# Kernel tuning notes

Measured on AMD Instinct MI355X. Metric: run time of the kernel, lower is better.

The kernel has to match this reference:

```python
import jax, jax.numpy as jnp
import numpy as np

# aero table grids (degrees)
A_LO, A_HI = -20.0, 90.0
B_LO, B_HI = -30.0, 30.0
E_LO, E_HI = -25.0, 25.0


def _idx(x, lo, hi, n):
    t = jnp.clip((x - lo) / (hi - lo) * (n - 1), 0.0, float(n - 1))
    i0 = jnp.clip(t.astype(jnp.int32), 0, n - 2)
    return i0, t - i0


def _interp1(tab, x, lo, hi):
    i0, f = _idx(x, lo, hi, tab.shape[-1])
    return tab[..., i0] * (1.0 - f) + tab[..., i0 + 1] * f


def _interp2(tab, a, b):
    ia, fa = _idx(a, A_LO, A_HI, tab.shape[-2])
    ib, fb = _idx(b, B_LO, B_HI, tab.shape[-1])
    return (tab[:, ia, ib] * (1 - fa) * (1 - fb)
            + tab[:, ia + 1, ib] * fa * (1 - fb)
            + tab[:, ia, ib + 1] * (1 - fa) * fb
            + tab[:, ia + 1, ib + 1] * fa * fb)


def _interp3(tab, a, b, e):
    ia, fa = _idx(a, A_LO, A_HI, tab.shape[-3])
    ib, fb = _idx(b, B_LO, B_HI, tab.shape[-2])
    ie, fe = _idx(e, E_LO, E_HI, tab.shape[-1])
    out = 0.0
    for di, wa in ((0, 1 - fa), (1, fa)):
        for dj, wb in ((0, 1 - fb), (1, fb)):
            for dk, we in ((0, 1 - fe), (1, fe)):
                out = out + tab[:, ia + di, ib + dj, ie + dk] * (wa * wb * we)
    return out


def _nlplant(xu, tab3, tab2, tab1, tab_eta):
    g, m, Bspan, S, cbar = 32.17, 636.94, 30.0, 300.0, 11.32
    xcgr, xcg, Heng = 0.35, 0.25, 0.0
    Jy, Jxz, Jz, Jx = 55814.0, 982.0, 63100.0, 9496.0
    r2d = 180.0 / np.pi

    alt = xu[:, 2]
    phi, theta, psi = xu[:, 3], xu[:, 4], xu[:, 5]
    vt = jnp.maximum(xu[:, 6], 0.01)          # if vt < 0.01: vt = 0.01
    alpha, beta = xu[:, 7], xu[:, 8]
    a_deg, b_deg = alpha * r2d, beta * r2d
    P, Q, R = xu[:, 9], xu[:, 10], xu[:, 11]
    T, el, ail, rud, lef = xu[:, 12], xu[:, 13], xu[:, 14], xu[:, 15], xu[:, 16]
    dail, drud, dlef = ail / 21.5, rud / 30.0, 1.0 - lef / 25.0

    # --- Atmos ---
    tfac = 1.0 - 7.03e-06 * alt
    temp = jnp.where(alt >= 35000.0, 390.0, 519.0 * tfac)
    rho = 0.002377 * jnp.power(tfac, 4.14)
    qbar = 0.5 * rho * vt * vt
    ps = 1715.0 * rho * temp
    ps = jnp.where(ps == 0.0, 1715.0, ps)

    sa, ca = jnp.sin(alpha), jnp.cos(alpha)
    sb, cb = jnp.sin(beta), jnp.cos(beta)
    st, ct, tt = jnp.sin(theta), jnp.cos(theta), jnp.tan(theta)
    sphi, cphi = jnp.sin(phi), jnp.cos(phi)
    spsi, cpsi = jnp.sin(psi), jnp.cos(psi)

    U, V, W = vt * ca * cb, vt * sb, vt * sa * cb

    xd0 = U * (ct * cpsi) + V * (sphi * cpsi * st - cphi * spsi) + W * (cphi * st * cpsi + sphi * spsi)
    xd1 = U * (ct * spsi) + V * (sphi * spsi * st + cphi * cpsi) + W * (cphi * st * spsi - sphi * cpsi)
    xd2 = U * st - V * (sphi * ct) - W * (cphi * ct)
    xd3 = P + tt * (Q * sphi + R * cphi)
    xd4 = Q * cphi - R * sphi
    xd5 = (Q * sphi + R * cphi) / ct

    # --- aero table lookups ---
    v3 = _interp3(tab3, a_deg, b_deg, el)                    # [5,B]: Cx,Cz,Cm,Cn,Cl at el
    v30 = _interp3(tab3, a_deg, b_deg, jnp.zeros_like(el))   # [5,B]: at el=0
    v2 = _interp2(tab2, a_deg, b_deg)                        # [16,B]
    v1 = _interp1(tab1, a_deg, A_LO, A_HI)                   # [21,B]
    eta_el = _interp1(tab_eta, el, E_LO, E_HI)               # [B]

    Cx, Cz, Cm, Cn, Cl = v3[0], v3[1], v3[2], v3[3], v3[4]
    Cy = v2[0]
    (Cxq, Cyr, Cyp, Czq, Clr, Clp, Cmq, Cnr, Cnp,
     dCxq_lef, dCyr_lef, dCyp_lef, dCzq_lef, dClr_lef, dClp_lef,
     dCmq_lef, dCnr_lef, dCnp_lef, dCnbeta, dClbeta, dCm) = [v1[i] for i in range(21)]

    d_Cx_lef = v2[1] - v30[0]
    d_Cz_lef = v2[2] - v30[1]
    d_Cm_lef = v2[3] - v30[2]
    d_Cy_lef = v2[4] - v2[0]
    d_Cn_lef = v2[5] - v30[3]
    d_Cl_lef = v2[6] - v30[4]
    d_Cy_r30 = v2[7] - v2[0]
    d_Cn_r30 = v2[8] - v30[3]
    d_Cl_r30 = v2[9] - v30[4]
    d_Cy_a20 = v2[10] - v2[0]
    d_Cy_a20_lef = v2[11] - v2[4]
    d_Cn_a20 = v2[12] - v30[3]
    d_Cn_a20_lef = v2[13] - v2[5]
    d_Cl_a20 = v2[14] - v30[4]
    d_Cl_a20_lef = v2[15] - v2[6]
    d_Cm_ds = 0.0

    # --- total coefficients ---
    c2v = 1.0 / (2.0 * vt)
    dXdQ = cbar * c2v * (Cxq + dCxq_lef * dlef)
    Cx_tot = Cx + d_Cx_lef * dlef + dXdQ * Q
    dZdQ = cbar * c2v * (Czq + dCzq_lef * dlef)
    Cz_tot = Cz + d_Cz_lef * dlef + dZdQ * Q
    dMdQ = cbar * c2v * (Cmq + dCmq_lef * dlef)
    Cm_tot = Cm * eta_el + Cz_tot * (xcgr - xcg) + d_Cm_lef * dlef + dMdQ * Q + dCm + d_Cm_ds
    dYdail = d_Cy_a20 + d_Cy_a20_lef * dlef
    dYdR = Bspan * c2v * (Cyr + dCyr_lef * dlef)
    dYdP = Bspan * c2v * (Cyp + dCyp_lef * dlef)
    Cy_tot = Cy + d_Cy_lef * dlef + dYdail * dail + d_Cy_r30 * drud + dYdR * R + dYdP * P
    dNdail = d_Cn_a20 + d_Cn_a20_lef * dlef
    dNdR = Bspan * c2v * (Cnr + dCnr_lef * dlef)
    dNdP = Bspan * c2v * (Cnp + dCnp_lef * dlef)
    Cn_tot = (Cn + d_Cn_lef * dlef - Cy_tot * (xcgr - xcg) * (cbar / Bspan)
              + dNdail * dail + d_Cn_r30 * drud + dNdR * R + dNdP * P + dCnbeta * b_deg)
    dLdail = d_Cl_a20 + d_Cl_a20_lef * dlef
    dLdR = Bspan * c2v * (Clr + dClr_lef * dlef)
    dLdP = Bspan * c2v * (Clp + dClp_lef * dlef)
    Cl_tot = (Cl + d_Cl_lef * dlef + dLdail * dail + d_Cl_r30 * drud
              + dLdR * R + dLdP * P + dClbeta * b_deg)

    # --- body-axis accelerations ---
    qS_m = qbar * S / m
    Udot = R * V - Q * W - g * st + qS_m * Cx_tot + T / m
    Vdot = P * W - R * U + g * ct * sphi + qS_m * Cy_tot
    Wdot = Q * U - P * V + g * ct * cphi + qS_m * Cz_tot
    vt_dot = (U * Udot + V * Vdot + W * Wdot) / vt
    alpha_dot = (U * Wdot - W * Udot) / (U * U + W * W)
    beta_dot = (Vdot * vt - V * vt_dot) / (vt * vt * cb)

    # --- moments ---
    L_tot = Cl_tot * qbar * S * Bspan
    M_tot = Cm_tot * qbar * S * cbar
    N_tot = Cn_tot * qbar * S * Bspan
    denom = Jx * Jz - Jxz * Jxz
    P_dot = (Jz * L_tot + Jxz * N_tot - (Jz * (Jz - Jy) + Jxz * Jxz) * Q * R
             + Jxz * (Jx - Jy + Jz) * P * Q + Jxz * Q * Heng) / denom
    Q_dot = (M_tot + (Jz - Jx) * P * R - Jxz * (P * P - R * R) - R * Heng) / Jy
    R_dot = (Jx * N_tot + Jxz * L_tot + (Jx * (Jx - Jy) + Jxz * Jxz) * P * Q
             - Jxz * (Jx - Jy + Jz) * Q * R + Jx * Q * Heng) / denom

    xdot12 = jnp.stack([xd0, xd1, xd2, xd3, xd4, xd5,
                        vt_dot, alpha_dot, beta_dot, P_dot, Q_dot, R_dot], axis=1)
    return jnp.concatenate([xdot12, jnp.zeros((xu.shape[0], 5), xu.dtype)], axis=1)


def setup_inputs() -> dict:
    key = jax.random.key(0)
    k0, k1, k2, k3, k4 = jax.random.split(key, 5)
    Bn = 1 << 20
    u = jax.random.uniform(k0, (Bn, 17), dtype=jnp.float32)
    lo = jnp.array([0., 0., 0., -1., -1., -3., 300., -0.30, -0.5, -2., -2., -2.,
                    1000., -25., -21.5, -30., 0.], dtype=jnp.float32)
    hi = jnp.array([1000., 1000., 40000., 1., 1., 3., 900., 0.75, 0.5, 2., 2., 2.,
                    19000., 25., 21.5, 30., 25.], dtype=jnp.float32)
    xu = lo + u * (hi - lo)
    tab3 = 0.1 * jax.random.normal(k1, (5, 20, 19, 5), dtype=jnp.float32)
    tab2 = 0.05 * jax.random.normal(k2, (16, 20, 19), dtype=jnp.float32)
    tab1 = 0.1 * jax.random.normal(k3, (21, 20), dtype=jnp.float32)
    tab_eta = 1.0 + 0.05 * jax.random.normal(k4, (5,), dtype=jnp.float32)
    return {"xu": xu, "tab3": tab3, "tab2": tab2, "tab1": tab1, "tab_eta": tab_eta}


def reference(xu, tab3, tab2, tab1, tab_eta):
    return _nlplant(xu, tab3, tab2, tab1, tab_eta)
```

## Files before the change

### kernel.cpp

```cpp
#include <hip/hip_runtime.h>

#define BLOCK 1024
#define ROWS_PER_BLOCK 1024

__device__ __forceinline__ void idx_of(float x, float lo, float inv_range_times_nm1,
                                       int n, int& i0, float& f) {
    float t = (x - lo) * inv_range_times_nm1;
    t = fminf(fmaxf(t, 0.0f), (float)(n - 1));
    int i = (int)t;
    if (i > n - 2) i = n - 2;
    i0 = i;
    f = t - (float)i;
}

__global__ __launch_bounds__(BLOCK, 1)
void nlplant_kernel(const float* __restrict__ xu,
                    const float* __restrict__ tab3,
                    const float* __restrict__ tab2,
                    const float* __restrict__ tab1,
                    const float* __restrict__ tab_eta,
                    float* __restrict__ out, int nrows)
{
    __shared__ __align__(16) float s_t3a[1900 * 4];
    __shared__ __align__(16) float s_t3b[1900];
    __shared__ __align__(16) float s_tab2[380 * 20];
    __shared__ __align__(16) float s_tab1[20 * 21];
    __shared__ __align__(16) float s_eta[8];
    __shared__ __align__(16) float s_io[512 * 17];

    const int tid = threadIdx.x;

    for (int k = tid; k < 9500; k += BLOCK) {
        int ie = k % 5; int r = k / 5;
        int ib = r % 19; r /= 19;
        int ia = r % 20; int c = r / 20;
        const int idx = (ia * 19 + ib) * 5 + ie;
        const float v = tab3[k];
        if (c < 4) s_t3a[(idx << 2) + c] = v;
        else       s_t3b[idx] = v;
    }
    for (int k = tid; k < 6080; k += BLOCK) {
        int ib = k % 19; int r = k / 19;
        int ia = r % 20; int c = r / 20;
        s_tab2[(ia * 19 + ib) * 20 + c] = tab2[k];
    }
    for (int k = tid; k < 420; k += BLOCK) {
        int ia = k % 20; int c = k / 20;
        s_tab1[ia * 21 + c] = tab1[k];
    }
    if (tid < 5) s_eta[tid] = tab_eta[tid];

    const int base = blockIdx.x * ROWS_PER_BLOCK;
    int remA = nrows - base;           if (remA < 0) remA = 0;
    const int rowsA = remA < 512 ? remA : 512;
    int remB = nrows - base - 512;     if (remB < 0) remB = 0;
    const int rowsB = remB < 512 ? remB : 512;

    if (rowsA == 512) {
        const float4* src = reinterpret_cast<const float4*>(xu + (size_t)base * 17);
        float4* dst = reinterpret_cast<float4*>(s_io);
        for (int k = tid; k < 2176; k += BLOCK) dst[k] = src[k];
    } else {
        for (int k = tid; k < rowsA * 17; k += BLOCK) s_io[k] = xu[(size_t)base * 17 + k];
    }
    __syncthreads();

    const int half = tid >> 9;
    const int l = tid & 511;
    const bool active = (half == 0) ? (l < rowsA) : (l < rowsB);

    float x[17];
#pragma unroll
    for (int j = 0; j < 17; ++j) x[j] = 1.0f;

    if (half == 0 && l < rowsA) {
#pragma unroll
        for (int j = 0; j < 17; ++j) x[j] = s_io[l * 17 + j];
    }
    __syncthreads();

    if (rowsB == 512) {
        const float4* src = reinterpret_cast<const float4*>(xu + (size_t)(base + 512) * 17);
        float4* dst = reinterpret_cast<float4*>(s_io);
        for (int k = tid; k < 2176; k += BLOCK) dst[k] = src[k];
    } else {
        for (int k = tid; k < rowsB * 17; k += BLOCK) s_io[k] = xu[(size_t)(base + 512) * 17 + k];
    }
    __syncthreads();
    if (half == 1 && l < rowsB) {
#pragma unroll
        for (int j = 0; j < 17; ++j) x[j] = s_io[l * 17 + j];
    }

    const float g = 32.17f, m_ = 636.94f, Bs = 30.0f, S = 300.0f, cbar = 11.32f;
    const float xcgr = 0.35f, xcg = 0.25f;
    const float Jy = 55814.0f, Jxz = 982.0f, Jz = 63100.0f, Jx = 9496.0f;
    const float r2d = 57.29577951308232f;

    const float alt = x[2], phi = x[3], theta = x[4], psi = x[5];
    const float vt = fmaxf(x[6], 0.01f);
    const float alpha = x[7], beta = x[8];
    const float a_deg = alpha * r2d, b_deg = beta * r2d;
    const float P = x[9], Q = x[10], R = x[11];
    const float T = x[12], el = x[13], ail = x[14], rud = x[15], lef = x[16];

    const float dail = ail * (1.0f / 21.5f);
    const float drud = rud * (1.0f / 30.0f);
    const float dlef = 1.0f - lef * (1.0f / 25.0f);

    const float tfac = 1.0f - 7.03e-6f * alt;
    const float rho = 0.002377f * __expf(4.14f * __logf(tfac));
    const float qbar = 0.5f * rho * vt * vt;

    float sa, ca, sb, cb, st, ct, sphi, cphi, spsi, cpsi;
    __sincosf(alpha, &sa, &ca);
    __sincosf(beta, &sb, &cb);
    __sincosf(theta, &st, &ct);
    __sincosf(phi, &sphi, &cphi);
    __sincosf(psi, &spsi, &cpsi);
    const float tt = st / ct;

    int ia, ib, ie; float fa, fb, fe;
    idx_of(a_deg, -20.0f, 19.0f / 110.0f, 20, ia, fa);
    idx_of(b_deg, -30.0f, 18.0f / 60.0f, 19, ib, fb);
    idx_of(el,    -25.0f,  4.0f / 50.0f,  5, ie, fe);

    const float wa[2] = {1.0f - fa, fa};
    const float wb[2] = {1.0f - fb, fb};
    const float we[2] = {1.0f - fe, fe};

    float v3c[5]  = {0, 0, 0, 0, 0};
    float v30c[5] = {0, 0, 0, 0, 0};
#pragma unroll
    for (int di = 0; di < 2; ++di) {
#pragma unroll
        for (int dj = 0; dj < 2; ++dj) {
            const float wab = wa[di] * wb[dj];
            const int pb = ((ia + di) * 19 + (ib + dj)) * 5;
#pragma unroll
            for (int dk = 0; dk < 2; ++dk) {
                const int idx = pb + ie + dk;
                const float4 q = *reinterpret_cast<const float4*>(&s_t3a[idx << 2]);
                const float q4 = s_t3b[idx];
                const float w = wab * we[dk];
                v3c[0] += q.x * w; v3c[1] += q.y * w; v3c[2] += q.z * w;
                v3c[3] += q.w * w; v3c[4] += q4 * w;
            }
            const int zidx = pb + 2;
            const float4 q0 = *reinterpret_cast<const float4*>(&s_t3a[zidx << 2]);
            const float q04 = s_t3b[zidx];
            v30c[0] += q0.x * wab; v30c[1] += q0.y * wab; v30c[2] += q0.z * wab;
            v30c[3] += q0.w * wab; v30c[4] += q04 * wab;
        }
    }

    float v2c[16];
    {
        const float w00 = wa[0] * wb[0], w01 = wa[0] * wb[1];
        const float w10 = wa[1] * wb[0], w11 = wa[1] * wb[1];
        const float4* p00 = reinterpret_cast<const float4*>(&s_tab2[(ia * 19 + ib) * 20]);
        const float4* p01 = reinterpret_cast<const float4*>(&s_tab2[(ia * 19 + ib + 1) * 20]);
        const float4* p10 = reinterpret_cast<const float4*>(&s_tab2[((ia + 1) * 19 + ib) * 20]);
        const float4* p11 = reinterpret_cast<const float4*>(&s_tab2[((ia + 1) * 19 + ib + 1) * 20]);
#pragma unroll
        for (int q = 0; q < 4; ++q) {
            const float4 a = p00[q], b = p01[q], c = p10[q], d = p11[q];
            v2c[4 * q + 0] = a.x * w00 + b.x * w01 + c.x * w10 + d.x * w11;
            v2c[4 * q + 1] = a.y * w00 + b.y * w01 + c.y * w10 + d.y * w11;
            v2c[4 * q + 2] = a.z * w00 + b.z * w01 + c.z * w10 + d.z * w11;
            v2c[4 * q + 3] = a.w * w00 + b.w * w01 + c.w * w10 + d.w * w11;
        }
    }

    float v1c[21];
    {
        const float* r0 = &s_tab1[ia * 21];
        const float* r1 = &s_tab1[(ia + 1) * 21];
#pragma unroll
        for (int c = 0; c < 21; ++c) v1c[c] = r0[c] * wa[0] + r1[c] * wa[1];
    }
    const float eta_el = s_eta[ie] * we[0] + s_eta[ie + 1] * we[1];

    const float Cx = v3c[0], Cz = v3c[1], Cm = v3c[2], Cn = v3c[3], Cl = v3c[4];
    const float Cy = v2c[0];
    const float Cxq = v1c[0], Cyr = v1c[1], Cyp = v1c[2], Czq = v1c[3], Clr = v1c[4];
    const float Clp = v1c[5], Cmq = v1c[6], Cnr = v1c[7], Cnp = v1c[8];
    const float dCxq_lef = v1c[9], dCyr_lef = v1c[10], dCyp_lef = v1c[11];
    const float dCzq_lef = v1c[12], dClr_lef = v1c[13], dClp_lef = v1c[14];
    const float dCmq_lef = v1c[15], dCnr_lef = v1c[16], dCnp_lef = v1c[17];
    const float dCnbeta = v1c[18], dClbeta = v1c[19], dCm = v1c[20];

    const float d_Cx_lef = v2c[1] - v30c[0];
    const float d_Cz_lef = v2c[2] - v30c[1];
    const float d_Cm_lef = v2c[3] - v30c[2];
    const float d_Cy_lef = v2c[4] - v2c[0];
    const float d_Cn_lef = v2c[5] - v30c[3];
    const float d_Cl_lef = v2c[6] - v30c[4];
    const float d_Cy_r30 = v2c[7] - v2c[0];
    const float d_Cn_r30 = v2c[8] - v30c[3];
    const float d_Cl_r30 = v2c[9] - v30c[4];
    const float d_Cy_a20 = v2c[10] - v2c[0];
    const float d_Cy_a20_lef = v2c[11] - v2c[4];
    const float d_Cn_a20 = v2c[12] - v30c[3];
    const float d_Cn_a20_lef = v2c[13] - v2c[5];
    const float d_Cl_a20 = v2c[14] - v30c[4];
    const float d_Cl_a20_lef = v2c[15] - v2c[6];

    const float U = vt * ca * cb, V = vt * sb, W = vt * sa * cb;
    const float o0 = U * (ct * cpsi) + V * (sphi * cpsi * st - cphi * spsi) + W * (cphi * st * cpsi + sphi * spsi);
    const float o1 = U * (ct * spsi) + V * (sphi * spsi * st + cphi * cpsi) + W * (cphi * st * spsi - sphi * cpsi);
    const float o2 = U * st - V * (sphi * ct) - W * (cphi * ct);
    const float o3 = P + tt * (Q * sphi + R * cphi);
    const float o4 = Q * cphi - R * sphi;
    const float o5 = (Q * sphi + R * cphi) / ct;

    const float c2v = 1.0f / (2.0f * vt);
    const float cq = cbar * c2v, bq = Bs * c2v;
    const float dXdQ = cq * (Cxq + dCxq_lef * dlef);
    const float Cx_tot = Cx + d_Cx_lef * dlef + dXdQ * Q;
    const float dZdQ = cq * (Czq + dCzq_lef * dlef);
    const float Cz_tot = Cz + d_Cz_lef * dlef + dZdQ * Q;
    const float dMdQ = cq * (Cmq + dCmq_lef * dlef);
    const float Cm_tot = Cm * eta_el + Cz_tot * (xcgr - xcg) + d_Cm_lef * dlef + dMdQ * Q + dCm;
    const float dYdail = d_Cy_a20 + d_Cy_a20_lef * dlef;
    const float dYdR = bq * (Cyr + dCyr_lef * dlef);
    const float dYdP = bq * (Cyp + dCyp_lef * dlef);
    const float Cy_tot = Cy + d_Cy_lef * dlef + dYdail * dail + d_Cy_r30 * drud + dYdR * R + dYdP * P;
    const float dNdail = d_Cn_a20 + d_Cn_a20_lef * dlef;
    const float dNdR = bq * (Cnr + dCnr_lef * dlef);
    const float dNdP = bq * (Cnp + dCnp_lef * dlef);
    const float Cn_tot = Cn + d_Cn_lef * dlef - Cy_tot * ((xcgr - xcg) * (cbar / Bs))
                       + dNdail * dail + d_Cn_r30 * drud + dNdR * R + dNdP * P + dCnbeta * b_deg;
    const float dLdail = d_Cl_a20 + d_Cl_a20_lef * dlef;
    const float dLdR = bq * (Clr + dClr_lef * dlef);
    const float dLdP = bq * (Clp + dClp_lef * dlef);
    const float Cl_tot = Cl + d_Cl_lef * dlef + dLdail * dail + d_Cl_r30 * drud
                       + dLdR * R + dLdP * P + dClbeta * b_deg;

    const float qS = qbar * S;
    const float qS_m = qS * (1.0f / m_);
    const float Udot = R * V - Q * W - g * st + qS_m * Cx_tot + T * (1.0f / m_);
    const float Vdot = P * W - R * U + g * ct * sphi + qS_m * Cy_tot;
    const float Wdot = Q * U - P * V + g * ct * cphi + qS_m * Cz_tot;
    const float o6 = (U * Udot + V * Vdot + W * Wdot) / vt;
    const float o7 = (U * Wdot - W * Udot) / (U * U + W * W);
    const float o8 = (Vdot * vt - V * o6) / (vt * vt * cb);

    const float L_tot = Cl_tot * qS * Bs;
    const float M_tot = Cm_tot * qS * cbar;
    const float N_tot = Cn_tot * qS * Bs;
    const float denom = Jx * Jz - Jxz * Jxz;
    const float inv_denom = 1.0f / denom;
    const float o9  = (Jz * L_tot + Jxz * N_tot - (Jz * (Jz - Jy) + Jxz * Jxz) * Q * R
                      + Jxz * (Jx - Jy + Jz) * P * Q) * inv_denom;
    const float o10 = (M_tot + (Jz - Jx) * P * R - Jxz * (P * P - R * R)) * (1.0f / Jy);
    const float o11 = (Jx * N_tot + Jxz * L_tot + (Jx * (Jx - Jy) + Jxz * Jxz) * P * Q
                      - Jxz * (Jx - Jy + Jz) * Q * R) * inv_denom;

    float o[17] = {o0, o1, o2, o3, o4, o5, o6, o7, o8, o9, o10, o11,
                   0.0f, 0.0f, 0.0f, 0.0f, 0.0f};

    __syncthreads();
    if (half == 0 && active) {
#pragma unroll
        for (int j = 0; j < 17; ++j) s_io[l * 17 + j] = o[j];
    }
    __syncthreads();
    if (rowsA == 512) {
        const float4* src = reinterpret_cast<const float4*>(s_io);
        float4* dst = reinterpret_cast<float4*>(out + (size_t)base * 17);
        for (int k = tid; k < 2176; k += BLOCK) dst[k] = src[k];
    } else {
        for (int k = tid; k < rowsA * 17; k += BLOCK) out[(size_t)base * 17 + k] = s_io[k];
    }
    __syncthreads();
    if (half == 1 && active) {
#pragma unroll
        for (int j = 0; j < 17; ++j) s_io[l * 17 + j] = o[j];
    }
    __syncthreads();
    if (rowsB == 512) {
        const float4* src = reinterpret_cast<const float4*>(s_io);
        float4* dst = reinterpret_cast<float4*>(out + (size_t)(base + 512) * 17);
        for (int k = tid; k < 2176; k += BLOCK) dst[k] = src[k];
    } else {
        for (int k = tid; k < rowsB * 17; k += BLOCK) out[(size_t)(base + 512) * 17 + k] = s_io[k];
    }
}

extern "C" void kernel_launch(void* const* d_in, const int* in_sizes, int n_in,
                              void* d_out, int out_size, void* d_ws, size_t ws_size,
                              hipStream_t stream) {
    const float* xu      = (const float*)d_in[0];
    const float* tab3    = (const float*)d_in[1];
    const float* tab2    = (const float*)d_in[2];
    const float* tab1    = (const float*)d_in[3];
    const float* tab_eta = (const float*)d_in[4];
    float* out = (float*)d_out;

    const int nrows = in_sizes[0] / 17;
    const int grid = (nrows + ROWS_PER_BLOCK - 1) / ROWS_PER_BLOCK;
    nlplant_kernel<<<grid, BLOCK, 0, stream>>>(xu, tab3, tab2, tab1, tab_eta, out, nrows);
}
```

Baseline: 69.35 us.

## Shrink shared staging to four 256-row phases and swizzle tab2 layout

Cuts the I/O staging buffer from 512 to 256 rows, processed in four phases, and packs tab2 into 16-float rows with a rotation swizzle. The eta table moves into the tab1 buffer. Together these lower LDS use per block, presumably so two blocks can share a CU, and the launch bound is raised to match. The swizzle is meant to cut LDS bank conflicts on the tab2 float4 reads. The cost is twice as many barrier-separated staging phases, so each block spends more time synchronising.

```diff
diff --git a/kernel.cpp b/kernel.cpp
--- a/kernel.cpp
+++ b/kernel.cpp
@@ -2,6 +2,7 @@
 
 #define BLOCK 1024
 #define ROWS_PER_BLOCK 1024
+#define PHASE 256
 
 __device__ __forceinline__ void idx_of(float x, float lo, float inv_range_times_nm1,
                                        int n, int& i0, float& f) {
@@ -13,7 +14,7 @@
     f = t - (float)i;
 }
 
-__global__ __launch_bounds__(BLOCK, 1)
+__global__ __launch_bounds__(BLOCK, 8)
 void nlplant_kernel(const float* __restrict__ xu,
                     const float* __restrict__ tab3,
                     const float* __restrict__ tab2,
@@ -23,10 +24,9 @@
 {
     __shared__ __align__(16) float s_t3a[1900 * 4];
     __shared__ __align__(16) float s_t3b[1900];
-    __shared__ __align__(16) float s_tab2[380 * 20];
-    __shared__ __align__(16) float s_tab1[20 * 21];
-    __shared__ __align__(16) float s_eta[8];
-    __shared__ __align__(16) float s_io[512 * 17];
+    __shared__ __align__(16) float s_tab2[380 * 16];
+    __shared__ __align__(16) float s_tab1[428];
+    __shared__ __align__(16) float s_io[PHASE * 17];
 
     const int tid = threadIdx.x;
 
@@ -42,54 +42,43 @@
     for (int k = tid; k < 6080; k += BLOCK) {
         int ib = k % 19; int r = k / 19;
         int ia = r % 20; int c = r / 20;
-        s_tab2[(ia * 19 + ib) * 20 + c] = tab2[k];
+        const int idx = ia * 19 + ib;
+        const int q = c >> 2, j = c & 3;
+        s_tab2[(idx << 4) + (((q + (idx >> 1)) & 3) << 2) + j] = tab2[k];
     }
     for (int k = tid; k < 420; k += BLOCK) {
         int ia = k % 20; int c = k / 20;
         s_tab1[ia * 21 + c] = tab1[k];
     }
-    if (tid < 5) s_eta[tid] = tab_eta[tid];
+    if (tid < 5) s_tab1[420 + tid] = tab_eta[tid];
 
     const int base = blockIdx.x * ROWS_PER_BLOCK;
-    int remA = nrows - base;           if (remA < 0) remA = 0;
-    const int rowsA = remA < 512 ? remA : 512;
-    int remB = nrows - base - 512;     if (remB < 0) remB = 0;
-    const int rowsB = remB < 512 ? remB : 512;
-
-    if (rowsA == 512) {
-        const float4* src = reinterpret_cast<const float4*>(xu + (size_t)base * 17);
-        float4* dst = reinterpret_cast<float4*>(s_io);
-        for (int k = tid; k < 2176; k += BLOCK) dst[k] = src[k];
-    } else {
-        for (int k = tid; k < rowsA * 17; k += BLOCK) s_io[k] = xu[(size_t)base * 17 + k];
-    }
-    __syncthreads();
-
-    const int half = tid >> 9;
-    const int l = tid & 511;
-    const bool active = (half == 0) ? (l < rowsA) : (l < rowsB);
+    const int own = tid >> 8;
+    const int l = tid & 255;
 
     float x[17];
 #pragma unroll
     for (int j = 0; j < 17; ++j) x[j] = 1.0f;
-
-    if (half == 0 && l < rowsA) {
-#pragma unroll
-        for (int j = 0; j < 17; ++j) x[j] = s_io[l * 17 + j];
-    }
-    __syncthreads();
-
-    if (rowsB == 512) {
-        const float4* src = reinterpret_cast<const float4*>(xu + (size_t)(base + 512) * 17);
-        float4* dst = reinterpret_cast<float4*>(s_io);
-        for (int k = tid; k < 2176; k += BLOCK) dst[k] = src[k];
-    } else {
-        for (int k = tid; k < rowsB * 17; k += BLOCK) s_io[k] = xu[(size_t)(base + 512) * 17 + k];
-    }
-    __syncthreads();
-    if (half == 1 && l < rowsB) {
-#pragma unroll
-        for (int j = 0; j < 17; ++j) x[j] = s_io[l * 17 + j];
+    bool active = false;
+
+    for (int p = 0; p < 4; ++p) {
+        const int pb = base + p * PHASE;
+        int rem = nrows - pb; if (rem < 0) rem = 0;
+        const int rows = rem < PHASE ? rem : PHASE;
+        if (rows == PHASE) {
+            const float4* src = reinterpret_cast<const float4*>(xu + (size_t)pb * 17);
+            float4* dst = reinterpret_cast<float4*>(s_io);
+            for (int k = tid; k < PHASE * 17 / 4; k += BLOCK) dst[k] = src[k];
+        } else {
+            for (int k = tid; k < rows * 17; k += BLOCK) s_io[k] = xu[(size_t)pb * 17 + k];
+        }
+        __syncthreads();
+        if (own == p && l < rows) {
+            active = true;
+#pragma unroll
+            for (int j = 0; j < 17; ++j) x[j] = s_io[l * 17 + j];
+        }
+        __syncthreads();
     }
 
     const float g = 32.17f, m_ = 636.94f, Bs = 30.0f, S = 300.0f, cbar = 11.32f;
@@ -136,17 +125,17 @@
 #pragma unroll
         for (int dj = 0; dj < 2; ++dj) {
             const float wab = wa[di] * wb[dj];
-            const int pb = ((ia + di) * 19 + (ib + dj)) * 5;
+            const int pb3 = ((ia + di) * 19 + (ib + dj)) * 5;
 #pragma unroll
             for (int dk = 0; dk < 2; ++dk) {
-                const int idx = pb + ie + dk;
+                const int idx = pb3 + ie + dk;
                 const float4 q = *reinterpret_cast<const float4*>(&s_t3a[idx << 2]);
                 const float q4 = s_t3b[idx];
                 const float w = wab * we[dk];
                 v3c[0] += q.x * w; v3c[1] += q.y * w; v3c[2] += q.z * w;
                 v3c[3] += q.w * w; v3c[4] += q4 * w;
             }
-            const int zidx = pb + 2;
+            const int zidx = pb3 + 2;
             const float4 q0 = *reinterpret_cast<const float4*>(&s_t3a[zidx << 2]);
             const float q04 = s_t3b[zidx];
             v30c[0] += q0.x * wab; v30c[1] += q0.y * wab; v30c[2] += q0.z * wab;
@@ -158,13 +147,17 @@
     {
         const float w00 = wa[0] * wb[0], w01 = wa[0] * wb[1];
         const float w10 = wa[1] * wb[0], w11 = wa[1] * wb[1];
-        const float4* p00 = reinterpret_cast<const float4*>(&s_tab2[(ia * 19 + ib) * 20]);
-        const float4* p01 = reinterpret_cast<const float4*>(&s_tab2[(ia * 19 + ib + 1) * 20]);
-        const float4* p10 = reinterpret_cast<const float4*>(&s_tab2[((ia + 1) * 19 + ib) * 20]);
-        const float4* p11 = reinterpret_cast<const float4*>(&s_tab2[((ia + 1) * 19 + ib + 1) * 20]);
+        const int i00 = ia * 19 + ib, i01 = i00 + 1, i10 = i00 + 19, i11 = i00 + 20;
+        const int b00 = i00 << 4, s00 = (i00 >> 1) & 3;
+        const int b01 = i01 << 4, s01 = (i01 >> 1) & 3;
+        const int b10 = i10 << 4, s10 = (i10 >> 1) & 3;
+        const int b11 = i11 << 4, s11 = (i11 >> 1) & 3;
 #pragma unroll
         for (int q = 0; q < 4; ++q) {
-            const float4 a = p00[q], b = p01[q], c = p10[q], d = p11[q];
+            const float4 a = *reinterpret_cast<const float4*>(&s_tab2[b00 + (((q + s00) & 3) << 2)]);
+            const float4 b = *reinterpret_cast<const float4*>(&s_tab2[b01 + (((q + s01) & 3) << 2)]);
+            const float4 c = *reinterpret_cast<const float4*>(&s_tab2[b10 + (((q + s10) & 3) << 2)]);
+            const float4 d = *reinterpret_cast<const float4*>(&s_tab2[b11 + (((q + s11) & 3) << 2)]);
             v2c[4 * q + 0] = a.x * w00 + b.x * w01 + c.x * w10 + d.x * w11;
             v2c[4 * q + 1] = a.y * w00 + b.y * w01 + c.y * w10 + d.y * w11;
             v2c[4 * q + 2] = a.z * w00 + b.z * w01 + c.z * w10 + d.z * w11;
@@ -179,7 +172,7 @@
 #pragma unroll
         for (int c = 0; c < 21; ++c) v1c[c] = r0[c] * wa[0] + r1[c] * wa[1];
     }
-    const float eta_el = s_eta[ie] * we[0] + s_eta[ie + 1] * we[1];
+    const float eta_el = s_tab1[420 + ie] * we[0] + s_tab1[421 + ie] * we[1];
 
     const float Cx = v3c[0], Cz = v3c[1], Cm = v3c[2], Cn = v3c[3], Cl = v3c[4];
     const float Cy = v2c[0];
@@ -260,31 +253,23 @@
     float o[17] = {o0, o1, o2, o3, o4, o5, o6, o7, o8, o9, o10, o11,
                    0.0f, 0.0f, 0.0f, 0.0f, 0.0f};
 
-    __syncthreads();
-    if (half == 0 && active) {
-#pragma unroll
-        for (int j = 0; j < 17; ++j) s_io[l * 17 + j] = o[j];
-    }
-    __syncthreads();
-    if (rowsA == 512) {
-        const float4* src = reinterpret_cast<const float4*>(s_io);
-        float4* dst = reinterpret_cast<float4*>(out + (size_t)base * 17);
-        for (int k = tid; k < 2176; k += BLOCK) dst[k] = src[k];
-    } else {
-        for (int k = tid; k < rowsA * 17; k += BLOCK) out[(size_t)base * 17 + k] = s_io[k];
-    }
-    __syncthreads();
-    if (half == 1 && active) {
-#pragma unroll
-        for (int j = 0; j < 17; ++j) s_io[l * 17 + j] = o[j];
-    }
-    __syncthreads();
-    if (rowsB == 512) {
-        const float4* src = reinterpret_cast<const float4*>(s_io);
-        float4* dst = reinterpret_cast<float4*>(out + (size_t)(base + 512) * 17);
-        for (int k = tid; k < 2176; k += BLOCK) dst[k] = src[k];
-    } else {
-        for (int k = tid; k < rowsB * 17; k += BLOCK) out[(size_t)(base + 512) * 17 + k] = s_io[k];
+    for (int p = 0; p < 4; ++p) {
+        const int pb = base + p * PHASE;
+        int rem = nrows - pb; if (rem < 0) rem = 0;
+        const int rows = rem < PHASE ? rem : PHASE;
+        if (own == p && active) {
+#pragma unroll
+            for (int j = 0; j < 17; ++j) s_io[l * 17 + j] = o[j];
+        }
+        __syncthreads();
+        if (rows == PHASE) {
+            const float4* src = reinterpret_cast<const float4*>(s_io);
+            float4* dst = reinterpret_cast<float4*>(out + (size_t)pb * 17);
+            for (int k = tid; k < PHASE * 17 / 4; k += BLOCK) dst[k] = src[k];
+        } else {
+            for (int k = tid; k < rows * 17; k += BLOCK) out[(size_t)pb * 17 + k] = s_io[k];
+        }
+        __syncthreads();
     }
 }
 
```

After: 239.0 us. 245% more time.
